# Performance work log

Measured on AMD Instinct MI355X. Metric: run time of the kernel, lower is better.

## Reference

```python
import jax, jax.numpy as jnp
import numpy as np


def setup_inputs() -> dict:
    key = jax.random.key(0)
    k1, k2, k3 = jax.random.split(key, 3)
    B, C, E, L, W = 4, 2, 256, 16000, 40
    mixture_w = jax.random.normal(k1, (B, E, L), dtype=jnp.float32)
    est_mask = jax.random.uniform(k2, (B, C, E, L), dtype=jnp.float32)
    basis_w = jax.random.normal(k3, (W, E), dtype=jnp.float32) * (1.0 / np.sqrt(E))
    return {"mixture_w": mixture_w, "est_mask": est_mask, "basis_w": basis_w}


def overlap_and_add(frames, frame_step):
    # frames: [B, C, L, W] -> [B, C, T] with T = (L-1)*frame_step + W
    B, C, L, W = frames.shape
    T = (L - 1) * frame_step + W
    # scatter-add each frame into the output waveform at its strided offset
    idx = (jnp.arange(L)[:, None] * frame_step + jnp.arange(W)[None, :]).reshape(-1)
    out = jnp.zeros((B, C, T), dtype=frames.dtype)
    return out.at[..., idx].add(frames.reshape(B, C, L * W))


def reference(mixture_w, est_mask, basis_w):
    # mixture_w: [B, E, L], est_mask: [B, C, E, L], basis_w: [W, E]
    source_w = mixture_w[:, None, :, :] * est_mask          # [B, C, E, L]
    # transpose(2,3) then Linear(E->W): contract over E
    est_frames = jnp.einsum('bcel,we->bclw', source_w, basis_w)  # [B, C, L, W]
    W = basis_w.shape[0]
    return overlap_and_add(est_frames, W // 2)              # [B, C, T]
```

## Files before the change

kernel.cpp:

```cpp
#include <hip/hip_runtime.h>

#define BQ   4
#define CQ   2
#define EQ   256
#define LQ   16000
#define WQ   40
#define STEP 20
#define TQ   ((LQ - 1) * STEP + WQ)
#define TLF  63
#define OWN  (TLF * STEP)
#define NBX  254
#define NH   8
#define EH   (EQ / NH)
#define NCP  4
#define SPAN (TLF * STEP + WQ + STEP)

__global__ void transpose_basis_kernel(const float* __restrict__ basis,
                                       float* __restrict__ wsT) {
    int i = blockIdx.x * 256 + threadIdx.x;
    if (i < EQ * WQ) {
        int e = i / WQ;
        int w = i - e * WQ;
        wsT[i] = basis[w * EQ + e];
    }
}

__global__ __launch_bounds__(512, 4) void decoder_kernel(
    const float* __restrict__ mix,
    const float* __restrict__ mask,
    const float* __restrict__ wsT,
    float* __restrict__ out)
{
    __shared__ float outS[NCP][CQ][SPAN];

    const int tid = threadIdx.x;
    const int ll  = tid & 63;
    const int h   = __builtin_amdgcn_readfirstlane(tid >> 6);
    const int bx  = blockIdx.x;
    const int b   = blockIdx.y;
    const int f   = TLF * bx - 1 + ll;

    const int   fc    = min(max(f, 0), LQ - 1);
    const float valid = (f >= 0 && f < LQ) ? 1.0f : 0.0f;

    float acc0[WQ], acc1[WQ];
#pragma unroll
    for (int w = 0; w < WQ; ++w) { acc0[w] = 0.0f; acc1[w] = 0.0f; }

    const float* mp  = mix  + ((size_t)b * EQ + h * EH) * LQ + fc;
    const float* kp0 = mask + (((size_t)(b * CQ)) * EQ + h * EH) * LQ + fc;
    const float* kp1 = kp0 + (size_t)EQ * LQ;
    const float* bp  = wsT + (size_t)h * EH * WQ;

    for (int eo = 0; eo < EH; eo += 2) {
        float m0  = mp[(size_t)eo * LQ];
        float m1  = mp[(size_t)(eo + 1) * LQ];
        float k00 = kp0[(size_t)eo * LQ] * valid;
        float k01 = kp0[(size_t)(eo + 1) * LQ] * valid;
        float k10 = kp1[(size_t)eo * LQ] * valid;
        float k11 = kp1[(size_t)(eo + 1) * LQ] * valid;
        {
            float s0 = m0 * k00;
            float s1 = m0 * k10;
            const float* bb = bp + eo * WQ;
#pragma unroll
            for (int w = 0; w < WQ; ++w) {
                acc0[w] = fmaf(s0, bb[w], acc0[w]);
                acc1[w] = fmaf(s1, bb[w], acc1[w]);
            }
        }
        {
            float s0 = m1 * k01;
            float s1 = m1 * k11;
            const float* bb = bp + (eo + 1) * WQ;
#pragma unroll
            for (int w = 0; w < WQ; ++w) {
                acc0[w] = fmaf(s0, bb[w], acc0[w]);
                acc1[w] = fmaf(s1, bb[w], acc1[w]);
            }
        }
    }

    const int base = ll * STEP;
    const int cp   = h >> 1;
    const int hp   = h & 1;
    if (hp == 0 && (ll & 1) == 0) {
#pragma unroll
        for (int w = 0; w < WQ; ++w) {
            outS[cp][0][base + w] = acc0[w];
            outS[cp][1][base + w] = acc1[w];
        }
    }
    __syncthreads();
    if (hp == 0 && (ll & 1) == 1) {
#pragma unroll
        for (int w = 0; w < WQ; ++w) {
            outS[cp][0][base + w] += acc0[w];
            outS[cp][1][base + w] += acc1[w];
        }
    }
    __syncthreads();
    if (hp == 1 && (ll & 1) == 0) {
#pragma unroll
        for (int w = 0; w < WQ; ++w) {
            outS[cp][0][base + w] += acc0[w];
            outS[cp][1][base + w] += acc1[w];
        }
    }
    __syncthreads();
    if (hp == 1 && (ll & 1) == 1) {
#pragma unroll
        for (int w = 0; w < WQ; ++w) {
            outS[cp][0][base + w] += acc0[w];
            outS[cp][1][base + w] += acc1[w];
        }
    }
    __syncthreads();

    for (int cc = 0; cc < CQ; ++cc) {
        const size_t ob = ((size_t)b * CQ + cc) * TQ + (size_t)OWN * bx;
        for (int i = tid; i < OWN; i += 512) {
            const long t = (long)OWN * bx + i;
            if (t < (long)TQ) {
                out[ob + i] = outS[0][cc][STEP + i] + outS[1][cc][STEP + i]
                            + outS[2][cc][STEP + i] + outS[3][cc][STEP + i];
            }
        }
    }
}

extern "C" void kernel_launch(void* const* d_in, const int* in_sizes, int n_in,
                              void* d_out, int out_size, void* d_ws, size_t ws_size,
                              hipStream_t stream) {
    const float* mix   = (const float*)d_in[0];
    const float* mask  = (const float*)d_in[1];
    const float* basis = (const float*)d_in[2];
    float* out = (float*)d_out;
    float* wsT = (float*)d_ws;

    transpose_basis_kernel<<<dim3((EQ * WQ + 255) / 256), 256, 0, stream>>>(basis, wsT);

    dim3 grid(NBX, BQ);
    decoder_kernel<<<grid, 512, 0, stream>>>(mix, mask, wsT, out);
}
```

Measured before the change: 244.5 us.

## Double-buffer mix/mask loads into LDS via async global_load_lds

Replaces direct per-thread global loads of mixture and mask rows with asynchronous global-to-LDS loads, double-buffered per wave in chunks of four embedding rows, so the next chunk's memory traffic overlaps the current chunk's FMAs. The staging buffer is unioned with the overlap-add shared buffer, and occupancy hint drops from 4 to 3 blocks per CU. Manual vmcnt waits and sched barriers are used for ordering. This risks extra LDS traffic and lower occupancy, and correctness relies on the hand-written waitcnt values.

```diff
diff --git a/kernel.cpp b/kernel.cpp
--- a/kernel.cpp
+++ b/kernel.cpp
@@ -12,8 +12,12 @@
 #define NBX  254
 #define NH   8
 #define EH   (EQ / NH)
+#define EC   4
+#define NCH  (EH / EC)
+#define SROWS (3 * EC)
 #define NCP  4
 #define SPAN (TLF * STEP + WQ + STEP)
+#define POOLF ((NH * 2 * SROWS * 64) > (NCP * CQ * SPAN) ? (NH * 2 * SROWS * 64) : (NCP * CQ * SPAN))
 
 __global__ void transpose_basis_kernel(const float* __restrict__ basis,
                                        float* __restrict__ wsT) {
@@ -25,44 +29,41 @@
     }
 }
 
-__global__ __launch_bounds__(512, 4) void decoder_kernel(
-    const float* __restrict__ mix,
-    const float* __restrict__ mask,
-    const float* __restrict__ wsT,
-    float* __restrict__ out)
-{
-    __shared__ float outS[NCP][CQ][SPAN];
+__device__ __forceinline__ void stage_chunk(const float* mpB, const float* kpB0,
+                                            const float* kpB1, float* dstBase,
+                                            int e0, int ll) {
+#pragma unroll
+    for (int r = 0; r < EC; ++r)
+        __builtin_amdgcn_global_load_lds(
+            (const __attribute__((address_space(1))) void*)(mpB + (size_t)(e0 + r) * LQ + ll),
+            (__attribute__((address_space(3))) void*)(dstBase + r * 64), 4, 0, 0);
+#pragma unroll
+    for (int r = 0; r < EC; ++r)
+        __builtin_amdgcn_global_load_lds(
+            (const __attribute__((address_space(1))) void*)(kpB0 + (size_t)(e0 + r) * LQ + ll),
+            (__attribute__((address_space(3))) void*)(dstBase + (EC + r) * 64), 4, 0, 0);
+#pragma unroll
+    for (int r = 0; r < EC; ++r)
+        __builtin_amdgcn_global_load_lds(
+            (const __attribute__((address_space(1))) void*)(kpB1 + (size_t)(e0 + r) * LQ + ll),
+            (__attribute__((address_space(3))) void*)(dstBase + (2 * EC + r) * 64), 4, 0, 0);
+}
 
-    const int tid = threadIdx.x;
-    const int ll  = tid & 63;
-    const int h   = __builtin_amdgcn_readfirstlane(tid >> 6);
-    const int bx  = blockIdx.x;
-    const int b   = blockIdx.y;
-    const int f   = TLF * bx - 1 + ll;
-
-    const int   fc    = min(max(f, 0), LQ - 1);
-    const float valid = (f >= 0 && f < LQ) ? 1.0f : 0.0f;
-
-    float acc0[WQ], acc1[WQ];
+__device__ __forceinline__ void compute_chunk(const float* sl, int idx, float valid,
+                                              const float* bbB,
+                                              float acc0[WQ], float acc1[WQ]) {
 #pragma unroll
-    for (int w = 0; w < WQ; ++w) { acc0[w] = 0.0f; acc1[w] = 0.0f; }
-
-    const float* mp  = mix  + ((size_t)b * EQ + h * EH) * LQ + fc;
-    const float* kp0 = mask + (((size_t)(b * CQ)) * EQ + h * EH) * LQ + fc;
-    const float* kp1 = kp0 + (size_t)EQ * LQ;
-    const float* bp  = wsT + (size_t)h * EH * WQ;
-
-    for (int eo = 0; eo < EH; eo += 2) {
-        float m0  = mp[(size_t)eo * LQ];
-        float m1  = mp[(size_t)(eo + 1) * LQ];
-        float k00 = kp0[(size_t)eo * LQ] * valid;
-        float k01 = kp0[(size_t)(eo + 1) * LQ] * valid;
-        float k10 = kp1[(size_t)eo * LQ] * valid;
-        float k11 = kp1[(size_t)(eo + 1) * LQ] * valid;
+    for (int eo = 0; eo < EC; eo += 2) {
+        float m0  = sl[(eo)*64 + idx];
+        float m1  = sl[(eo + 1)*64 + idx];
+        float k00 = sl[(EC + eo)*64 + idx] * valid;
+        float k01 = sl[(EC + eo + 1)*64 + idx] * valid;
+        float k10 = sl[(2*EC + eo)*64 + idx] * valid;
+        float k11 = sl[(2*EC + eo + 1)*64 + idx] * valid;
         {
             float s0 = m0 * k00;
             float s1 = m0 * k10;
-            const float* bb = bp + eo * WQ;
+            const float* bb = bbB + eo * WQ;
 #pragma unroll
             for (int w = 0; w < WQ; ++w) {
                 acc0[w] = fmaf(s0, bb[w], acc0[w]);
@@ -72,7 +73,7 @@
         {
             float s0 = m1 * k01;
             float s1 = m1 * k11;
-            const float* bb = bp + (eo + 1) * WQ;
+            const float* bb = bbB + (eo + 1) * WQ;
 #pragma unroll
             for (int w = 0; w < WQ; ++w) {
                 acc0[w] = fmaf(s0, bb[w], acc0[w]);
@@ -80,6 +81,57 @@
             }
         }
     }
+}
+
+__global__ __launch_bounds__(512, 3) void decoder_kernel(
+    const float* __restrict__ mix,
+    const float* __restrict__ mask,
+    const float* __restrict__ wsT,
+    float* __restrict__ out)
+{
+    __shared__ float poolF[POOLF];
+
+    const int tid = threadIdx.x;
+    const int ll  = tid & 63;
+    const int h   = __builtin_amdgcn_readfirstlane(tid >> 6);
+    const int bx  = blockIdx.x;
+    const int b   = blockIdx.y;
+    const int f0  = TLF * bx - 1;
+    const int f   = f0 + ll;
+
+    const int   f0c   = min(max(f0, 0), LQ - 64);
+    const int   fc    = min(max(f, 0), LQ - 1);
+    const int   idx   = fc - f0c;
+    const float valid = (f >= 0 && f < LQ) ? 1.0f : 0.0f;
+
+    float acc0[WQ], acc1[WQ];
+#pragma unroll
+    for (int w = 0; w < WQ; ++w) { acc0[w] = 0.0f; acc1[w] = 0.0f; }
+
+    const float* mpB  = mix  + ((size_t)b * EQ + h * EH) * LQ + f0c;
+    const float* kpB0 = mask + (((size_t)(b * CQ)) * EQ + h * EH) * LQ + f0c;
+    const float* kpB1 = kpB0 + (size_t)EQ * LQ;
+    const float* bp   = wsT + (size_t)h * EH * WQ;
+
+    float* myStage0 = poolF + (h * 2 + 0) * (SROWS * 64);
+    float* myStage1 = poolF + (h * 2 + 1) * (SROWS * 64);
+
+    stage_chunk(mpB, kpB0, kpB1, myStage0, 0, ll);
+#pragma unroll 1
+    for (int t = 0; t < NCH - 1; ++t) {
+        float* nxt = ((t + 1) & 1) ? myStage1 : myStage0;
+        stage_chunk(mpB, kpB0, kpB1, nxt, (t + 1) * EC, ll);
+        asm volatile("s_waitcnt vmcnt(12)" ::: "memory");
+        __builtin_amdgcn_sched_barrier(0);
+        const float* cur = (t & 1) ? myStage1 : myStage0;
+        compute_chunk(cur, idx, valid, bp + t * EC * WQ, acc0, acc1);
+    }
+    asm volatile("s_waitcnt vmcnt(0)" ::: "memory");
+    __builtin_amdgcn_sched_barrier(0);
+    compute_chunk(myStage1, idx, valid, bp + (NCH - 1) * EC * WQ, acc0, acc1);
+
+    __syncthreads();
+    float (*outS)[CQ][SPAN] = (float (*)[CQ][SPAN])poolF;
 
     const int base = ll * STEP;
     const int cp   = h >> 1;
```

After: 243.0 us. About the same (-0.6%).
